# Performance work log

Measured on AMD Instinct MI355X. Metric: run time of the kernel, lower is better.

Reference implementation:

```python
import jax, jax.numpy as jnp
import numpy as np

N = 50000      # total nodes in batched graph
E = 800000     # total edges
G = 256        # number of graphs in batch
IN_DIM = 32
HID = 108      # hidden_dim == out_dim
N_CLASSES = 10
L = 4          # number of GraphSage layers
EPS = 1e-12


def setup_inputs() -> dict:
    key = jax.random.key(0)
    ks = jax.random.split(key, 20)
    s = 0.05
    inp = {
        'nodes_feat': jax.random.normal(ks[0], (N, IN_DIM), jnp.float32),
        'edges_feat': jax.random.normal(ks[1], (E, 1), jnp.float32),
        'nodes_num_norm_sqrt': jax.random.uniform(ks[2], (N, 1), jnp.float32),
        'edges_num_norm_sqrt': jax.random.uniform(ks[3], (E, 1), jnp.float32),
        'src': jax.random.randint(ks[4], (E,), 0, N, jnp.int32),
        'dst': jax.random.randint(ks[5], (E,), 0, N, jnp.int32),
        'graph_ids': jnp.sort(jax.random.randint(ks[6], (N,), 0, G, jnp.int32)),
        # parameters
        'W_emb': jax.random.normal(ks[7], (IN_DIM, HID), jnp.float32) * s,
        'b_emb': jnp.zeros((HID,), jnp.float32),
        'W_pool': jax.random.normal(ks[8], (L, HID, HID), jnp.float32) * s,
        'b_pool': jnp.zeros((L, HID), jnp.float32),
        'W_app': jax.random.normal(ks[9], (L, 2 * HID, HID), jnp.float32) * s,
        'b_app': jnp.zeros((L, HID), jnp.float32),
        'W_mlp1': jax.random.normal(ks[10], (HID, HID // 2), jnp.float32) * s,
        'b_mlp1': jnp.zeros((HID // 2,), jnp.float32),
        'W_mlp2': jax.random.normal(ks[11], (HID // 2, HID // 4), jnp.float32) * s,
        'b_mlp2': jnp.zeros((HID // 4,), jnp.float32),
        'W_mlp3': jax.random.normal(ks[12], (HID // 4, N_CLASSES), jnp.float32) * s,
        'b_mlp3': jnp.zeros((N_CLASSES,), jnp.float32),
    }
    return inp


def _l2norm(x):
    # F.normalize(x, p=2, dim=1)
    n = jnp.sqrt(jnp.sum(x * x, axis=1, keepdims=True))
    return x / jnp.maximum(n, EPS)


def reference(nodes_feat, edges_feat, nodes_num_norm_sqrt, edges_num_norm_sqrt,
              src, dst, graph_ids,
              W_emb, b_emb, W_pool, b_pool, W_app, b_app,
              W_mlp1, b_mlp1, W_mlp2, b_mlp2, W_mlp3, b_mlp3):
    # input embedding (dropout p=0 -> identity)
    h = nodes_feat @ W_emb + b_emb  # [N, HID]

    # in-degree per node (constant across layers)
    deg = jax.ops.segment_sum(jnp.ones((E,), h.dtype), dst, num_segments=N)
    inv_deg = (1.0 / jnp.maximum(deg, 1.0))[:, None]  # zero in-degree -> agg 0

    for l in range(L):
        h_in = h
        # meanpool aggregator: per-source linear+relu, mean over in-neighbors
        h_pool = jax.nn.relu(h @ W_pool[l] + b_pool[l])  # [N, HID]
        agg = jax.ops.segment_sum(h_pool[src], dst, num_segments=N) * inv_deg
        # NodeApply: concat(self, agg) -> linear -> L2 normalize -> relu
        bundle = jnp.concatenate([h, agg], axis=1) @ W_app[l] + b_app[l]
        h = jax.nn.relu(_l2norm(bundle))
        h = h_in + h  # residual (in_dim == out_dim for all layers)

    # dgl.mean_nodes readout over ragged graphs
    hg_sum = jax.ops.segment_sum(h, graph_ids, num_segments=G)  # [G, HID]
    cnt = jax.ops.segment_sum(jnp.ones((N,), h.dtype), graph_ids, num_segments=G)
    hg = hg_sum / jnp.maximum(cnt, 1.0)[:, None]

    # MLPReadout: 108 -> 54 -> 27 -> 10
    y = jax.nn.relu(hg @ W_mlp1 + b_mlp1)
    y = jax.nn.relu(y @ W_mlp2 + b_mlp2)
    logits = y @ W_mlp3 + b_mlp3  # [G, N_CLASSES]
    return logits
```

## Files before the change

### kernel.cpp

```cpp
#include <hip/hip_runtime.h>

#define NN 50000
#define EE 800000
#define GG 256
#define IND 32
#define HID 108
#define NL 4
#define MB 782
#define RS 8
#define SBN 196
#define SCAP 5120
#define PCAP 6144
#define PAD 16
#define BCH 4096
#define STL 136

typedef __attribute__((ext_vector_type(8))) _Float16 f16x8;
typedef __attribute__((ext_vector_type(4))) float floatx4;
typedef __attribute__((ext_vector_type(4))) unsigned int uintx4;

__global__ void k_zero(int* p, int n) {
    int i = blockIdx.x * 256 + threadIdx.x;
    if (i < n) p[i] = 0;
}

__global__ __launch_bounds__(256)
void k_bin(const int* __restrict__ src, const int* __restrict__ dst,
           int* __restrict__ gfill, unsigned int* __restrict__ ebuf) {
    __shared__ unsigned int stage[BCH];
    __shared__ int scnt[SBN], soff[SBN], gres[SBN];
    int tid = threadIdx.x;
    int e0 = blockIdx.x * BCH;
    for (int i = tid; i < SBN; i += 256) scnt[i] = 0;
    __syncthreads();
    unsigned int pay[16]; int psb[16];
    #pragma unroll
    for (int j = 0; j < 16; j++) {
        int e = e0 + j * 256 + tid;
        if (e < EE) {
            int d = dst[e]; int s = src[e];
            int sb = d >> 8;
            psb[j] = sb;
            pay[j] = ((unsigned)sb << 24) | ((unsigned)s << 8) | (unsigned)(d & 255);
            atomicAdd(&scnt[sb], 1);
        } else psb[j] = -1;
    }
    __syncthreads();
    if (tid == 0) {
        int run = 0;
        for (int s = 0; s < SBN; s++) { soff[s] = run; run += scnt[s]; }
    }
    __syncthreads();
    if (tid < SBN) gres[tid] = atomicAdd(&gfill[tid * PAD], scnt[tid]);
    __syncthreads();
    if (tid < SBN) scnt[tid] = 0;
    __syncthreads();
    #pragma unroll
    for (int j = 0; j < 16; j++) {
        if (psb[j] >= 0) {
            int p = soff[psb[j]] + atomicAdd(&scnt[psb[j]], 1);
            stage[p] = pay[j];
        }
    }
    __syncthreads();
    int nv = soff[SBN - 1] + scnt[SBN - 1];
    for (int i = tid; i < nv; i += 256) {
        unsigned int v = stage[i];
        int sb = v >> 24;
        int idx = gres[sb] + (i - soff[sb]);
        if (idx < SCAP) ebuf[(size_t)sb * SCAP + idx] = v & 0xFFFFFFu;
    }
}

__global__ __launch_bounds__(256)
void k_place2(const unsigned int* __restrict__ ebuf, const int* __restrict__ gfill,
              int* __restrict__ rp, unsigned short* __restrict__ cs) {
    __shared__ int outb[PCAP];
    __shared__ int cnt[256];
    __shared__ int off[256];
    __shared__ int fl[SBN];
    __shared__ int sbase;
    __shared__ int wsum[4], wexc[4];
    int sb = blockIdx.x, tid = threadIdx.x;
    if (tid < SBN) fl[tid] = gfill[tid * PAD];
    cnt[tid] = 0;
    __syncthreads();
    if (tid == 0) {
        int run = 0;
        for (int s = 0; s < sb; s++) run += fl[s];
        sbase = run;
    }
    __syncthreads();
    int nE = fl[sb]; if (nE > SCAP) nE = SCAP;
    int base = sbase;
    const unsigned int* eb = ebuf + (size_t)sb * SCAP;
    for (int i = tid; i < nE; i += 256) atomicAdd(&cnt[eb[i] & 255], 1);
    __syncthreads();
    int v = cnt[tid];
    int lane = tid & 63, wv = tid >> 6;
    int x = v;
    #pragma unroll
    for (int o = 1; o < 64; o <<= 1) {
        int y = __shfl_up(x, o, 64);
        if (lane >= o) x += y;
    }
    if (lane == 63) wsum[wv] = x;
    __syncthreads();
    if (tid == 0) { int run = 0; for (int w = 0; w < 4; w++) { wexc[w] = run; run += wsum[w]; } }
    __syncthreads();
    int myoff = wexc[wv] + x - v;
    off[tid] = myoff;
    int n = (sb << 8) + tid;
    if (n <= NN) rp[n] = base + myoff;
    cnt[tid] = 0;
    __syncthreads();
    if (nE <= PCAP) {
        for (int i = tid; i < nE; i += 256) {
            unsigned int e = eb[i];
            int loc = e & 255;
            int p = atomicAdd(&cnt[loc], 1);
            outb[off[loc] + p] = (int)(e >> 8);
        }
        __syncthreads();
        for (int i = tid; i < nE; i += 256) cs[base + i] = (unsigned short)outb[i];
    } else {
        for (int i = tid; i < nE; i += 256) {
            unsigned int e = eb[i];
            int loc = e & 255;
            int p = atomicAdd(&cnt[loc], 1);
            cs[base + off[loc] + p] = (unsigned short)(e >> 8);
        }
    }
}

__global__ void k_pack(const float* __restrict__ W_pool, const float* __restrict__ b_pool,
                       const float* __restrict__ W_app, const float* __restrict__ b_app,
                       const float* __restrict__ W_emb, const float* __restrict__ b_emb,
                       _Float16* Bt1, _Float16* BtA, float* bbP, float* bbA,
                       _Float16* BtE, float* bbE) {
    int r = blockIdx.x * 256 + threadIdx.x;
    if (r < NL * 128 * 128) {
        int l = r / (128 * 128); int t = r % (128 * 128); int n = t / 128, k = t % 128;
        float v = (n < HID && k < HID) ? W_pool[((size_t)l * HID + k) * HID + n] : 0.f;
        Bt1[r] = (_Float16)v; return;
    } r -= NL * 128 * 128;
    if (r < NL * 108 * 256) {
        int l = r / (108 * 256); int t = r % (108 * 256); int n = t / 256, k = t % 256;
        float v = 0.f;
        if (k < HID)                        v = W_app[((size_t)l * 216 + k) * HID + n];
        else if (k >= 128 && k < 128 + HID) v = W_app[((size_t)l * 216 + 108 + (k - 128)) * HID + n];
        BtA[r] = (_Float16)v; return;
    } r -= NL * 108 * 256;
    if (r < NL * 128) { int l = r / 128, n = r % 128; bbP[r] = (n < HID) ? b_pool[l * HID + n] : 0.f; return; } r -= NL * 128;
    if (r < NL * 128) { int l = r / 128, n = r % 128; bbA[r] = (n < HID) ? b_app[l * HID + n] : 0.f; return; } r -= NL * 128;
    if (r < 128 * 32) {
        int n = r / 32, k = r % 32;
        BtE[r] = (n < HID) ? (_Float16)W_emb[k * HID + n] : (_Float16)0.f; return;
    } r -= 128 * 32;
    if (r < 128) { bbE[r] = (r < HID) ? b_emb[r] : 0.f; }
}

__global__ __launch_bounds__(256)
void k_embed2(const float* __restrict__ feat, const _Float16* __restrict__ BtE,
              const float* __restrict__ bias,
              const _Float16* __restrict__ Bt1n, const float* __restrict__ bbPn,
              float* __restrict__ h, _Float16* __restrict__ h16,
              _Float16* __restrict__ hp16) {
    __shared__ _Float16 Bl[128 * 32];
    __shared__ _Float16 stg[64 * STL];
    int tid = threadIdx.x;
    for (int i = tid; i < 128 * 32 / 8; i += 256)
        ((uintx4*)Bl)[i] = ((const uintx4*)BtE)[i];
    __syncthreads();
    int lane = tid & 63, wid = tid >> 6, lm = lane & 15, lq = lane >> 4;
    int m0 = blockIdx.x * 64;
    floatx4 acc[4][2];
    #pragma unroll
    for (int mi = 0; mi < 4; mi++)
        #pragma unroll
        for (int ni = 0; ni < 2; ni++) { floatx4 z = {0.f,0.f,0.f,0.f}; acc[mi][ni] = z; }
    f16x8 a[4], b[2];
    #pragma unroll
    for (int mi = 0; mi < 4; mi++) {
        int row = m0 + mi * 16 + lm;
        f16x8 av;
        if (row < NN) {
            const float4 v0 = *(const float4*)(feat + (size_t)row * 32 + lq * 8);
            const float4 v1 = *(const float4*)(feat + (size_t)row * 32 + lq * 8 + 4);
            av[0] = (_Float16)v0.x; av[1] = (_Float16)v0.y;
            av[2] = (_Float16)v0.z; av[3] = (_Float16)v0.w;
            av[4] = (_Float16)v1.x; av[5] = (_Float16)v1.y;
            av[6] = (_Float16)v1.z; av[7] = (_Float16)v1.w;
        } else {
            #pragma unroll
            for (int j = 0; j < 8; j++) av[j] = (_Float16)0.f;
        }
        a[mi] = av;
    }
    #pragma unroll
    for (int ni = 0; ni < 2; ni++) {
        int col = wid * 32 + ni * 16 + lm;
        b[ni] = *(const f16x8*)&Bl[col * 32 + lq * 8];
    }
    #pragma unroll
    for (int mi = 0; mi < 4; mi++)
        #pragma unroll
        for (int ni = 0; ni < 2; ni++)
            acc[mi][ni] = __builtin_amdgcn_mfma_f32_16x16x32_f16(a[mi], b[ni], acc[mi][ni], 0, 0, 0);
    #pragma unroll
    for (int mi = 0; mi < 4; mi++)
        #pragma unroll
        for (int ni = 0; ni < 2; ni++) {
            int col = wid * 32 + ni * 16 + lm;
            float bc = bias[col];
            #pragma unroll
            for (int r = 0; r < 4; r++) {
                int rl = mi * 16 + lq * 4 + r;
                int row = m0 + rl;
                float v = acc[mi][ni][r] + bc;
                stg[rl * STL + col] = (_Float16)v;
                if (row < NN) {
                    h16[(size_t)row * 128 + col] = (_Float16)v;
                    if (col < HID) h[(size_t)row * HID + col] = v;
                }
            }
        }
    __syncthreads();
    floatx4 pacc[4][2];
    #pragma unroll
    for (int mi = 0; mi < 4; mi++)
        #pragma unroll
        for (int ni = 0; ni < 2; ni++) { floatx4 z = {0.f,0.f,0.f,0.f}; pacc[mi][ni] = z; }
    #pragma unroll
    for (int ks = 0; ks < 4; ks++) {
        f16x8 pa[4], pb[2];
        #pragma unroll
        for (int mi = 0; mi < 4; mi++)
            pa[mi] = *(const f16x8*)&stg[(mi * 16 + lm) * STL + ks * 32 + lq * 8];
        #pragma unroll
        for (int ni = 0; ni < 2; ni++)
            pb[ni] = *(const f16x8*)(Bt1n + (size_t)(wid * 32 + ni * 16 + lm) * 128 + ks * 32 + lq * 8);
        #pragma unroll
        for (int mi = 0; mi < 4; mi++)
            #pragma unroll
            for (int ni = 0; ni < 2; ni++)
                pacc[mi][ni] = __builtin_amdgcn_mfma_f32_16x16x32_f16(pa[mi], pb[ni], pacc[mi][ni], 0, 0, 0);
    }
    #pragma unroll
    for (int mi = 0; mi < 4; mi++)
        #pragma unroll
        for (int ni = 0; ni < 2; ni++) {
            int col = wid * 32 + ni * 16 + lm;
            float bc = bbPn[col];
            #pragma unroll
            for (int r = 0; r < 4; r++) {
                int row = m0 + mi * 16 + lq * 4 + r;
                if (row < NN)
                    hp16[(size_t)row * 128 + col] = (_Float16)fmaxf(pacc[mi][ni][r] + bc, 0.f);
            }
        }
}

__global__ __launch_bounds__(256)
void k_agg3(const _Float16* __restrict__ hp16, const int* __restrict__ rp,
            const unsigned short* __restrict__ cs, _Float16* __restrict__ agg16) {
    int bid = blockIdx.x;
    int bkt = bid >> 2;
    int slice = bid & 3;
    int tid = threadIdx.x;
    int wv = tid >> 6, lane = tid & 63;
    int nsub = lane >> 2, c = lane & 3;
    int n = bkt * 64 + wv * 16 + nsub;
    if (n < NN) {
        int s0 = rp[n], s1 = rp[n + 1];
        float acc[8];
        #pragma unroll
        for (int j = 0; j < 8; j++) acc[j] = 0.f;
        const _Float16* hb = hp16 + (size_t)slice * 32 + c * 8;
        int e = s0;
        for (; e + 4 <= s1; e += 4) {
            int r0 = __builtin_nontemporal_load(cs + e);
            int r1 = __builtin_nontemporal_load(cs + e + 1);
            int r2 = __builtin_nontemporal_load(cs + e + 2);
            int r3 = __builtin_nontemporal_load(cs + e + 3);
            f16x8 v0 = *(const f16x8*)(hb + (size_t)r0 * 128);
            f16x8 v1 = *(const f16x8*)(hb + (size_t)r1 * 128);
            f16x8 v2 = *(const f16x8*)(hb + (size_t)r2 * 128);
            f16x8 v3 = *(const f16x8*)(hb + (size_t)r3 * 128);
            #pragma unroll
            for (int j = 0; j < 8; j++)
                acc[j] += ((float)v0[j] + (float)v1[j]) + ((float)v2[j] + (float)v3[j]);
        }
        for (; e < s1; e++) {
            int r0 = __builtin_nontemporal_load(cs + e);
            f16x8 v0 = *(const f16x8*)(hb + (size_t)r0 * 128);
            #pragma unroll
            for (int j = 0; j < 8; j++) acc[j] += (float)v0[j];
        }
        int dg = s1 - s0;
        float inv = 1.0f / (float)((dg > 1) ? dg : 1);
        f16x8 o;
        #pragma unroll
        for (int j = 0; j < 8; j++) o[j] = (_Float16)(acc[j] * inv);
        uintx4 ov = *(uintx4*)&o;
        __builtin_nontemporal_store(ov, (uintx4*)(agg16 + (size_t)n * 128 + slice * 32 + c * 8));
    }
}

__global__ __launch_bounds__(256)
void k_appmm1(const _Float16* __restrict__ Ah, const _Float16* __restrict__ Ag,
              const _Float16* __restrict__ Bt, const float* __restrict__ bias,
              const _Float16* __restrict__ Bt1n, const float* __restrict__ bbPn,
              float* __restrict__ h, _Float16* __restrict__ h16,
              _Float16* __restrict__ hp16, int do_mm1) {
    __shared__ float ssl[64 * 4];
    __shared__ float scl[64];
    __shared__ _Float16 stg[64 * STL];
    int tid = threadIdx.x;
    int lane = tid & 63, wid = tid >> 6, lm = lane & 15, lq = lane >> 4;
    int m0 = blockIdx.x * 64;
    floatx4 acc[4][2];
    #pragma unroll
    for (int mi = 0; mi < 4; mi++)
        #pragma unroll
        for (int ni = 0; ni < 2; ni++) { floatx4 z = {0.f,0.f,0.f,0.f}; acc[mi][ni] = z; }
    f16x8 zf = {(_Float16)0, (_Float16)0, (_Float16)0, (_Float16)0,
                (_Float16)0, (_Float16)0, (_Float16)0, (_Float16)0};
    int colc[2], cval[2];
    #pragma unroll
    for (int ni = 0; ni < 2; ni++) {
        int col = wid * 32 + ni * 16 + lm;
        cval[ni] = (col < HID);
        colc[ni] = cval[ni] ? col : 0;
    }
    #pragma unroll
    for (int ks = 0; ks < 8; ks++) {
        const _Float16* Asrc = (ks < 4) ? Ah : Ag;
        int ko = (ks & 3) * 32 + lq * 8;
        f16x8 a[4], b[2];
        #pragma unroll
        for (int mi = 0; mi < 4; mi++) {
            int row = m0 + mi * 16 + lm;
            a[mi] = (row < NN) ? *(const f16x8*)(Asrc + (size_t)row * 128 + ko) : zf;
        }
        #pragma unroll
        for (int ni = 0; ni < 2; ni++)
            b[ni] = *(const f16x8*)(Bt + (size_t)colc[ni] * 256 + ks * 32 + lq * 8);
        #pragma unroll
        for (int mi = 0; mi < 4; mi++)
            #pragma unroll
            for (int ni = 0; ni < 2; ni++)
                acc[mi][ni] = __builtin_amdgcn_mfma_f32_16x16x32_f16(a[mi], b[ni], acc[mi][ni], 0, 0, 0);
    }
    #pragma unroll
    for (int ni = 0; ni < 2; ni++) {
        int col = wid * 32 + ni * 16 + lm;
        float bc = bias[col];
        #pragma unroll
        for (int mi = 0; mi < 4; mi++)
            #pragma unroll
            for (int r = 0; r < 4; r++) acc[mi][ni][r] += bc;
    }
    float ss[4][4];
    #pragma unroll
    for (int mi = 0; mi < 4; mi++)
        #pragma unroll
        for (int r = 0; r < 4; r++) {
            float c0 = cval[0] ? acc[mi][0][r] : 0.f;
            float c1 = cval[1] ? acc[mi][1][r] : 0.f;
            ss[mi][r] = c0 * c0 + c1 * c1;
        }
    #pragma unroll
    for (int off = 1; off < 16; off <<= 1)
        #pragma unroll
        for (int mi = 0; mi < 4; mi++)
            #pragma unroll
            for (int r = 0; r < 4; r++)
                ss[mi][r] += __shfl_xor(ss[mi][r], off, 64);
    if (lm == 0) {
        #pragma unroll
        for (int mi = 0; mi < 4; mi++)
            #pragma unroll
            for (int r = 0; r < 4; r++)
                ssl[(mi * 16 + lq * 4 + r) * 4 + wid] = ss[mi][r];
    }
    __syncthreads();
    if (tid < 64) {
        float s = ssl[tid * 4] + ssl[tid * 4 + 1] + ssl[tid * 4 + 2] + ssl[tid * 4 + 3];
        scl[tid] = 1.0f / fmaxf(sqrtf(s), 1e-12f);
    }
    __syncthreads();
    #pragma unroll
    for (int mi = 0; mi < 4; mi++)
        #pragma unroll
        for (int ni = 0; ni < 2; ni++) {
            int col = wid * 32 + ni * 16 + lm;
            #pragma unroll
            for (int r = 0; r < 4; r++) {
                int rl = mi * 16 + lq * 4 + r;
                int row = m0 + rl;
                float hn = 0.f;
                if (cval[ni] && row < NN) {
                    float v = fmaxf(acc[mi][ni][r] * scl[rl], 0.f);
                    hn = h[(size_t)row * HID + col] + v;
                    h[(size_t)row * HID + col] = hn;
                    h16[(size_t)row * 128 + col] = (_Float16)hn;
                }
                stg[rl * STL + col] = (_Float16)hn;
            }
        }
    if (do_mm1) {
        __syncthreads();
        floatx4 pacc[4][2];
        #pragma unroll
        for (int mi = 0; mi < 4; mi++)
            #pragma unroll
            for (int ni = 0; ni < 2; ni++) { floatx4 z = {0.f,0.f,0.f,0.f}; pacc[mi][ni] = z; }
        #pragma unroll
        for (int ks = 0; ks < 4; ks++) {
            f16x8 pa[4], pb[2];
            #pragma unroll
            for (int mi = 0; mi < 4; mi++)
                pa[mi] = *(const f16x8*)&stg[(mi * 16 + lm) * STL + ks * 32 + lq * 8];
            #pragma unroll
            for (int ni = 0; ni < 2; ni++)
                pb[ni] = *(const f16x8*)(Bt1n + (size_t)(wid * 32 + ni * 16 + lm) * 128 + ks * 32 + lq * 8);
            #pragma unroll
            for (int mi = 0; mi < 4; mi++)
                #pragma unroll
                for (int ni = 0; ni < 2; ni++)
                    pacc[mi][ni] = __builtin_amdgcn_mfma_f32_16x16x32_f16(pa[mi], pb[ni], pacc[mi][ni], 0, 0, 0);
        }
        #pragma unroll
        for (int mi = 0; mi < 4; mi++)
            #pragma unroll
            for (int ni = 0; ni < 2; ni++) {
                int col = wid * 32 + ni * 16 + lm;
                float bc = bbPn[col];
                #pragma unroll
                for (int r = 0; r < 4; r++) {
                    int row = m0 + mi * 16 + lq * 4 + r;
                    if (row < NN)
                        hp16[(size_t)row * 128 + col] = (_Float16)fmaxf(pacc[mi][ni][r] + bc, 0.f);
                }
            }
    }
}

__global__ __launch_bounds__(128)
void k_seg(const float* __restrict__ h, const int* __restrict__ gid,
           float* __restrict__ hgp) {
    __shared__ int se[2];
    int g = blockIdx.x, sl = blockIdx.y, tid = threadIdx.x;
    if (tid < 2) {
        int key = g + tid, lo = 0, hi = NN;
        while (lo < hi) {
            int mid = (lo + hi) >> 1;
            if (gid[mid] < key) lo = mid + 1; else hi = mid;
        }
        se[tid] = lo;
    }
    __syncthreads();
    int s = se[0], e = se[1];
    int cnt = e - s;
    int chunk = (cnt + RS - 1) / RS;
    int ls = s + sl * chunk;
    int le = min(e, ls + chunk);
    if (tid < HID) {
        float acc = 0.f;
        for (int n = ls; n < le; n++) acc += h[(size_t)n * HID + tid];
        hgp[((size_t)g * RS + sl) * HID + tid] = acc;
    }
}

__global__ __launch_bounds__(128)
void k_mlp(const float* __restrict__ hgp, const int* __restrict__ gid,
           const float* __restrict__ W1, const float* __restrict__ b1,
           const float* __restrict__ W2, const float* __restrict__ b2,
           const float* __restrict__ W3, const float* __restrict__ b3,
           float* __restrict__ out) {
    __shared__ float hg[HID];
    __shared__ float y1[54];
    __shared__ float y2[27];
    __shared__ int se[2];
    int g = blockIdx.x, tid = threadIdx.x;
    if (tid < 2) {
        int key = g + tid, lo = 0, hi = NN;
        while (lo < hi) {
            int mid = (lo + hi) >> 1;
            if (gid[mid] < key) lo = mid + 1; else hi = mid;
        }
        se[tid] = lo;
    }
    __syncthreads();
    int cnt = se[1] - se[0];
    if (tid < HID) {
        float acc = 0.f;
        #pragma unroll
        for (int sl = 0; sl < RS; sl++) acc += hgp[((size_t)g * RS + sl) * HID + tid];
        hg[tid] = acc / (float)((cnt > 1) ? cnt : 1);
    }
    __syncthreads();
    if (tid < 54) {
        float a = b1[tid];
        for (int k = 0; k < HID; k++) a += hg[k] * W1[k * 54 + tid];
        y1[tid] = fmaxf(a, 0.f);
    }
    __syncthreads();
    if (tid < 27) {
        float a = b2[tid];
        for (int k = 0; k < 54; k++) a += y1[k] * W2[k * 27 + tid];
        y2[tid] = fmaxf(a, 0.f);
    }
    __syncthreads();
    if (tid < 10) {
        float a = b3[tid];
        for (int k = 0; k < 27; k++) a += y2[k] * W3[k * 10 + tid];
        out[g * 10 + tid] = a;
    }
}

extern "C" void kernel_launch(void* const* d_in, const int* in_sizes, int n_in,
                              void* d_out, int out_size, void* d_ws, size_t ws_size,
                              hipStream_t stream) {
    float* out = (float*)d_out;
    (void)in_sizes; (void)n_in; (void)ws_size; (void)out_size;

    const float* feat   = (const float*)d_in[0];
    const int*   src    = (const int*)d_in[4];
    const int*   dst    = (const int*)d_in[5];
    const int*   gid    = (const int*)d_in[6];
    const float* W_emb  = (const float*)d_in[7];
    const float* b_emb  = (const float*)d_in[8];
    const float* W_pool = (const float*)d_in[9];
    const float* b_pool = (const float*)d_in[10];
    const float* W_app  = (const float*)d_in[11];
    const float* b_app  = (const float*)d_in[12];
    const float* W1     = (const float*)d_in[13];
    const float* b1     = (const float*)d_in[14];
    const float* W2     = (const float*)d_in[15];
    const float* b2     = (const float*)d_in[16];
    const float* W3     = (const float*)d_in[17];
    const float* b3     = (const float*)d_in[18];

    char* ws = (char*)d_ws;
    size_t off = 0;
    auto take = [&](size_t bytes) { char* p = ws + off; off += (bytes + 255) & ~(size_t)255; return p; };
    float*     h     = (float*)take((size_t)NN * HID * 4);
    _Float16*  h16   = (_Float16*)take((size_t)NN * 128 * 2);
    _Float16*  hp16  = (_Float16*)take((size_t)NN * 128 * 2);
    _Float16*  agg16 = (_Float16*)take((size_t)NN * 128 * 2);
    unsigned short* cs = (unsigned short*)take((size_t)EE * 2);
    unsigned int* ebuf = (unsigned int*)take((size_t)SBN * SCAP * 4);
    int*       rp    = (int*)take((size_t)(NN + 1) * 4);
    int*       gfill = (int*)take((size_t)SBN * PAD * 4);
    float*     hgp   = (float*)take((size_t)GG * RS * HID * 4);
    _Float16*  Bt1   = (_Float16*)take((size_t)NL * 128 * 128 * 2);
    _Float16*  BtA   = (_Float16*)take((size_t)NL * 108 * 256 * 2);
    float*     bbP   = (float*)take((size_t)NL * 128 * 4);
    float*     bbA   = (float*)take((size_t)NL * 128 * 4);
    _Float16*  BtE   = (_Float16*)take((size_t)128 * 32 * 2);
    float*     bbE   = (float*)take((size_t)128 * 4);

    hipLaunchKernelGGL(k_zero, dim3((SBN * PAD + 255) / 256), dim3(256), 0, stream,
                       gfill, SBN * PAD);
    hipLaunchKernelGGL(k_bin, dim3((EE + BCH - 1) / BCH), dim3(256), 0, stream,
                       src, dst, gfill, ebuf);
    hipLaunchKernelGGL(k_place2, dim3(SBN), dim3(256), 0, stream, ebuf, gfill, rp, cs);

    const int PACK_TOTAL = NL * 128 * 128 + NL * 108 * 256 + NL * 128 + NL * 128 + 128 * 32 + 128;
    hipLaunchKernelGGL(k_pack, dim3((PACK_TOTAL + 255) / 256), dim3(256), 0, stream,
                       W_pool, b_pool, W_app, b_app, W_emb, b_emb,
                       Bt1, BtA, bbP, bbA, BtE, bbE);

    hipLaunchKernelGGL(k_embed2, dim3(MB), dim3(256), 0, stream,
                       feat, BtE, bbE, Bt1, bbP, h, h16, hp16);

    for (int l = 0; l < NL; l++) {
        hipLaunchKernelGGL(k_agg3, dim3(4 * MB), dim3(256), 0, stream,
                           hp16, rp, cs, agg16);
        int next = (l + 1 < NL) ? 1 : 0;
        hipLaunchKernelGGL(k_appmm1, dim3(MB), dim3(256), 0, stream,
                           h16, agg16, BtA + (size_t)l * 108 * 256, bbA + (size_t)l * 128,
                           Bt1 + (size_t)(l + 1 < NL ? l + 1 : 0) * 128 * 128,
                           bbP + (size_t)(l + 1 < NL ? l + 1 : 0) * 128,
                           h, h16, hp16, next);
    }
    hipLaunchKernelGGL(k_seg, dim3(GG, RS), dim3(128), 0, stream, h, gid, hgp);
    hipLaunchKernelGGL(k_mlp, dim3(GG), dim3(128), 0, stream,
                       hgp, gid, W1, b1, W2, b2, W3, b3, out);
}
```

Before: 514.8 us.

## Halve appmm1 row tile to 32, raise occupancy, prefetch residual h early

```diff
diff --git a/kernel.cpp b/kernel.cpp
--- a/kernel.cpp
+++ b/kernel.cpp
@@ -7,6 +7,7 @@
 #define HID 108
 #define NL 4
 #define MB 782
+#define MB2 1563
 #define RS 8
 #define SBN 196
 #define SCAP 5120
@@ -307,29 +308,30 @@
     }
 }
 
-__global__ __launch_bounds__(256)
+__global__ __launch_bounds__(256, 6)
 void k_appmm1(const _Float16* __restrict__ Ah, const _Float16* __restrict__ Ag,
               const _Float16* __restrict__ Bt, const float* __restrict__ bias,
               const _Float16* __restrict__ Bt1n, const float* __restrict__ bbPn,
               float* __restrict__ h, _Float16* __restrict__ h16,
               _Float16* __restrict__ hp16, int do_mm1) {
-    __shared__ float ssl[64 * 4];
-    __shared__ float scl[64];
-    __shared__ _Float16 stg[64 * STL];
+    __shared__ float ssl[32 * 4];
+    __shared__ float scl[32];
+    __shared__ _Float16 stg[32 * STL];
     int tid = threadIdx.x;
     int lane = tid & 63, wid = tid >> 6, lm = lane & 15, lq = lane >> 4;
-    int m0 = blockIdx.x * 64;
-    floatx4 acc[4][2];
-    #pragma unroll
-    for (int mi = 0; mi < 4; mi++)
+    int m0 = blockIdx.x * 32;
+    floatx4 acc[2][2];
+    #pragma unroll
+    for (int mi = 0; mi < 2; mi++)
         #pragma unroll
         for (int ni = 0; ni < 2; ni++) { floatx4 z = {0.f,0.f,0.f,0.f}; acc[mi][ni] = z; }
     f16x8 zf = {(_Float16)0, (_Float16)0, (_Float16)0, (_Float16)0,
                 (_Float16)0, (_Float16)0, (_Float16)0, (_Float16)0};
-    int colc[2], cval[2];
+    int colv[2], colc[2], cval[2];
     #pragma unroll
     for (int ni = 0; ni < 2; ni++) {
         int col = wid * 32 + ni * 16 + lm;
+        colv[ni] = col;
         cval[ni] = (col < HID);
         colc[ni] = cval[ni] ? col : 0;
     }
@@ -337,9 +339,9 @@
     for (int ks = 0; ks < 8; ks++) {
         const _Float16* Asrc = (ks < 4) ? Ah : Ag;
         int ko = (ks & 3) * 32 + lq * 8;
-        f16x8 a[4], b[2];
-        #pragma unroll
-        for (int mi = 0; mi < 4; mi++) {
+        f16x8 a[2], b[2];
+        #pragma unroll
+        for (int mi = 0; mi < 2; mi++) {
             int row = m0 + mi * 16 + lm;
             a[mi] = (row < NN) ? *(const f16x8*)(Asrc + (size_t)row * 128 + ko) : zf;
         }
@@ -347,25 +349,30 @@
         for (int ni = 0; ni < 2; ni++)
             b[ni] = *(const f16x8*)(Bt + (size_t)colc[ni] * 256 + ks * 32 + lq * 8);
         #pragma unroll
-        for (int mi = 0; mi < 4; mi++)
+        for (int mi = 0; mi < 2; mi++)
             #pragma unroll
             for (int ni = 0; ni < 2; ni++)
                 acc[mi][ni] = __builtin_amdgcn_mfma_f32_16x16x32_f16(a[mi], b[ni], acc[mi][ni], 0, 0, 0);
     }
-    #pragma unroll
-    for (int ni = 0; ni < 2; ni++) {
-        int col = wid * 32 + ni * 16 + lm;
-        float bc = bias[col];
-        #pragma unroll
-        for (int mi = 0; mi < 4; mi++)
-            #pragma unroll
-            for (int r = 0; r < 4; r++) acc[mi][ni][r] += bc;
-    }
-    float ss[4][4];
-    #pragma unroll
-    for (int mi = 0; mi < 4; mi++)
+    float hres[2][2][4];
+    #pragma unroll
+    for (int mi = 0; mi < 2; mi++)
+        #pragma unroll
+        for (int ni = 0; ni < 2; ni++)
+            #pragma unroll
+            for (int r = 0; r < 4; r++) {
+                int row = m0 + mi * 16 + lq * 4 + r;
+                hres[mi][ni][r] = (cval[ni] && row < NN) ? h[(size_t)row * HID + colv[ni]] : 0.f;
+            }
+    float ss[2][4];
+    #pragma unroll
+    for (int mi = 0; mi < 2; mi++)
         #pragma unroll
         for (int r = 0; r < 4; r++) {
+            float bc0 = bias[colv[0]];
+            float bc1 = bias[colv[1]];
+            acc[mi][0][r] += bc0;
+            acc[mi][1][r] += bc1;
             float c0 = cval[0] ? acc[mi][0][r] : 0.f;
             float c1 = cval[1] ? acc[mi][1][r] : 0.f;
             ss[mi][r] = c0 * c0 + c1 * c1;
@@ -373,28 +380,28 @@
     #pragma unroll
     for (int off = 1; off < 16; off <<= 1)
         #pragma unroll
-        for (int mi = 0; mi < 4; mi++)
+        for (int mi = 0; mi < 2; mi++)
             #pragma unroll
             for (int r = 0; r < 4; r++)
                 ss[mi][r] += __shfl_xor(ss[mi][r], off, 64);
     if (lm == 0) {
         #pragma unroll
-        for (int mi = 0; mi < 4; mi++)
+        for (int mi = 0; mi < 2; mi++)
             #pragma unroll
             for (int r = 0; r < 4; r++)
                 ssl[(mi * 16 + lq * 4 + r) * 4 + wid] = ss[mi][r];
     }
     __syncthreads();
-    if (tid < 64) {
+    if (tid < 32) {
         float s = ssl[tid * 4] + ssl[tid * 4 + 1] + ssl[tid * 4 + 2] + ssl[tid * 4 + 3];
         scl[tid] = 1.0f / fmaxf(sqrtf(s), 1e-12f);
     }
     __syncthreads();
     #pragma unroll
-    for (int mi = 0; mi < 4; mi++)
+    for (int mi = 0; mi < 2; mi++)
         #pragma unroll
         for (int ni = 0; ni < 2; ni++) {
-            int col = wid * 32 + ni * 16 + lm;
+            int col = colv[ni];
             #pragma unroll
             for (int r = 0; r < 4; r++) {
                 int rl = mi * 16 + lq * 4 + r;
@@ -402,7 +409,7 @@
                 float hn = 0.f;
                 if (cval[ni] && row < NN) {
                     float v = fmaxf(acc[mi][ni][r] * scl[rl], 0.f);
-                    hn = h[(size_t)row * HID + col] + v;
+                    hn = hres[mi][ni][r] + v;
                     h[(size_t)row * HID + col] = hn;
                     h16[(size_t)row * 128 + col] = (_Float16)hn;
                 }
@@ -411,37 +418,36 @@
         }
     if (do_mm1) {
         __syncthreads();
-        floatx4 pacc[4][2];
-        #pragma unroll
-        for (int mi = 0; mi < 4; mi++)
+        floatx4 pacc[2][2];
+        #pragma unroll
+        for (int mi = 0; mi < 2; mi++)
             #pragma unroll
             for (int ni = 0; ni < 2; ni++) { floatx4 z = {0.f,0.f,0.f,0.f}; pacc[mi][ni] = z; }
         #pragma unroll
         for (int ks = 0; ks < 4; ks++) {
-            f16x8 pa[4], pb[2];
-            #pragma unroll
-            for (int mi = 0; mi < 4; mi++)
+            f16x8 pa[2], pb[2];
+            #pragma unroll
+            for (int mi = 0; mi < 2; mi++)
                 pa[mi] = *(const f16x8*)&stg[(mi * 16 + lm) * STL + ks * 32 + lq * 8];
             #pragma unroll
             for (int ni = 0; ni < 2; ni++)
-                pb[ni] = *(const f16x8*)(Bt1n + (size_t)(wid * 32 + ni * 16 + lm) * 128 + ks * 32 + lq * 8);
-            #pragma unroll
-            for (int mi = 0; mi < 4; mi++)
+                pb[ni] = *(const f16x8*)(Bt1n + (size_t)colv[ni] * 128 + ks * 32 + lq * 8);
+            #pragma unroll
+            for (int mi = 0; mi < 2; mi++)
                 #pragma unroll
                 for (int ni = 0; ni < 2; ni++)
                     pacc[mi][ni] = __builtin_amdgcn_mfma_f32_16x16x32_f16(pa[mi], pb[ni], pacc[mi][ni], 0, 0, 0);
         }
         #pragma unroll
-        for (int mi = 0; mi < 4; mi++)
+        for (int mi = 0; mi < 2; mi++)
             #pragma unroll
             for (int ni = 0; ni < 2; ni++) {
-                int col = wid * 32 + ni * 16 + lm;
-                float bc = bbPn[col];
+                float bc = bbPn[colv[ni]];
                 #pragma unroll
                 for (int r = 0; r < 4; r++) {
                     int row = m0 + mi * 16 + lq * 4 + r;
                     if (row < NN)
-                        hp16[(size_t)row * 128 + col] = (_Float16)fmaxf(pacc[mi][ni][r] + bc, 0.f);
+                        hp16[(size_t)row * 128 + colv[ni]] = (_Float16)fmaxf(pacc[mi][ni][r] + bc, 0.f);
                 }
             }
     }
@@ -580,7 +586,7 @@
         hipLaunchKernelGGL(k_agg3, dim3(4 * MB), dim3(256), 0, stream,
                            hp16, rp, cs, agg16);
         int next = (l + 1 < NL) ? 1 : 0;
-        hipLaunchKernelGGL(k_appmm1, dim3(MB), dim3(256), 0, stream,
+        hipLaunchKernelGGL(k_appmm1, dim3(MB2), dim3(256), 0, stream,
                            h16, agg16, BtA + (size_t)l * 108 * 256, bbA + (size_t)l * 128,
                            Bt1 + (size_t)(l + 1 < NL ? l + 1 : 0) * 128 * 128,
                            bbP + (size_t)(l + 1 < NL ? l + 1 : 0) * 128,
```

After: 517.6 us. No clear change (+0.6%).
